# Kernel tuning notes

Hardware: AMD Instinct MI355X
Metric: run time of the kernel (lower is better)

The kernel has to match this reference:

```python
import jax, jax.numpy as jnp
import numpy as np

B, N, H = 32, 2048, 128


def _lstm_step(c, h, x, Wi, Wh, b):
    # flax LSTMCell: gates i,f,g,o; sigmoid/sigmoid/tanh/sigmoid
    gates = x @ Wi + h @ Wh + b  # (B,N,4H)
    i, f, g, o = jnp.split(gates, 4, axis=-1)
    c_new = jax.nn.sigmoid(f) * c + jax.nn.sigmoid(i) * jnp.tanh(g)
    h_new = jax.nn.sigmoid(o) * jnp.tanh(c_new)
    return c_new, h_new


def setup_inputs() -> dict:
    key = jax.random.key(0)
    ks = jax.random.split(key, 24)
    f32 = jnp.float32
    inp = {}
    inp['node_embeddings'] = jax.random.normal(ks[0], (B, N, H), f32)
    for nm, k in zip(['hs_c0', 'hs_h0', 'hs_c1', 'hs_h1'], ks[1:5]):
        inp[nm] = jax.random.normal(k, (B, N, H), f32)
    ip = jax.random.uniform(ks[5], (B, N), f32)
    inp['instruction_pointer'] = ip / jnp.sum(ip, axis=-1, keepdims=True)
    inp['Wi0'] = jax.random.normal(ks[6], (H, 4 * H), f32) * 0.05
    inp['Wh0'] = jax.random.normal(ks[7], (H, 4 * H), f32) * 0.05
    inp['b0'] = jnp.zeros((4 * H,), f32)
    inp['Wi1'] = jax.random.normal(ks[8], (H, 4 * H), f32) * 0.05
    inp['Wh1'] = jax.random.normal(ks[9], (H, 4 * H), f32) * 0.05
    inp['b1'] = jnp.zeros((4 * H,), f32)
    inp['W_raise'] = jax.random.normal(ks[10], (4 * H, 2), f32) * 0.05
    inp['b_raise'] = jnp.zeros((2,), f32)
    inp['W_branch'] = jax.random.normal(ks[11], (4 * H, 2), f32) * 0.05
    inp['b_branch'] = jnp.zeros((2,), f32)
    inp['true_indexes'] = jax.random.randint(ks[12], (B, N), 0, N, jnp.int32)
    inp['false_indexes'] = jax.random.randint(ks[13], (B, N), 0, N, jnp.int32)
    inp['raise_indexes'] = jax.random.randint(ks[14], (B, N), 0, N, jnp.int32)
    inp['exit_node_indexes'] = jax.random.randint(ks[15], (B,), 0, N, jnp.int32)
    inp['raise_node_indexes'] = jax.random.randint(ks[16], (B,), 0, N, jnp.int32)
    inp['step_limits'] = jax.random.randint(ks[17], (B,), 0, 100, jnp.int32)
    inp['current_step'] = 5
    return inp


def reference(node_embeddings, hs_c0, hs_h0, hs_c1, hs_h1, instruction_pointer,
              Wi0, Wh0, b0, Wi1, Wh1, b1, W_raise, b_raise, W_branch, b_branch,
              true_indexes, false_indexes, raise_indexes,
              exit_node_indexes, raise_node_indexes, step_limits, current_step):
    bidx = jnp.arange(B)
    old = [hs_c0, hs_h0, hs_c1, hs_h1]

    # execute: per-node 2-layer stacked LSTM (vectorized over B,N)
    c0n, h0n = _lstm_step(hs_c0, hs_h0, node_embeddings, Wi0, Wh0, b0)
    c1n, h1n = _lstm_step(hs_c1, hs_h1, h0n, Wi1, Wh1, b1)
    contrib = [c0n, h0n, c1n, h1n]

    # mask_h: keep old state at exit node and (raise_in_ipagnn) at raise node
    def mask_nodes(hc, ho, idx):
        return hc.at[bidx, idx].set(ho[bidx, idx])
    contrib = [mask_nodes(mask_nodes(hc, ho, exit_node_indexes), ho, raise_node_indexes)
               for hc, ho in zip(contrib, old)]

    hs_emb = jnp.concatenate(contrib, axis=-1)  # (B,N,4H)

    raise_dec = jax.nn.softmax(hs_emb @ W_raise + b_raise, axis=-1)
    zero_one = jnp.array([0.0, 1.0], dtype=raise_dec.dtype)
    raise_dec = raise_dec.at[bidx, exit_node_indexes].set(zero_one)
    raise_dec = raise_dec.at[bidx, raise_node_indexes].set(zero_one)
    branch_dec = jax.nn.softmax(hs_emb @ W_branch + b_branch, axis=-1)

    p_raise = raise_dec[..., 0]
    p_noraise = raise_dec[..., 1]
    p_true = p_noraise * branch_dec[..., 0]
    p_false = p_noraise * branch_dec[..., 1]

    seg = jax.vmap(lambda v, idx: jax.ops.segment_sum(v, idx, num_segments=N))
    ip = instruction_pointer
    ip_new = (seg(p_raise * ip, raise_indexes)
              + seg(p_true * ip, true_indexes)
              + seg(p_false * ip, false_indexes))  # (B,N)
    denom = (ip_new + 1e-7)[..., None]

    wr = (p_raise * ip)[..., None]
    wt = (p_true * ip)[..., None]
    wf = (p_false * ip)[..., None]

    def agg(h):
        return (seg(h * wr, raise_indexes) + seg(h * wt, true_indexes)
                + seg(h * wf, false_indexes)) / denom
    hs_new = [agg(h) for h in contrib]

    # keep_old_if_done
    not_done = (current_step < step_limits)  # (B,)
    hs_out = [jnp.where(not_done[:, None, None], hn, ho) for hn, ho in zip(hs_new, old)]
    ip_out = jnp.where(not_done[:, None], ip_new, ip)

    # pack carry: (c0,h0,c1,h1, instruction_pointer) -> (B,N,4H+1)
    return jnp.concatenate(hs_out + [ip_out[..., None]], axis=-1)
```

## Files before the change

kernel.cpp:

```cpp
#include <hip/hip_runtime.h>
#include <stdint.h>

#define BB 32
#define NN 2048
#define HH 128
#define BN (BB*NN)

typedef short v8s __attribute__((ext_vector_type(8)));
typedef float v4f __attribute__((ext_vector_type(4)));

__device__ __forceinline__ unsigned short f2b(float f){
  union { float f; unsigned int i; } v; v.f = f;
  unsigned int x = v.i;
  unsigned int r = x + 0x7FFFu + ((x >> 16) & 1u);
  return (unsigned short)(r >> 16);
}
__device__ __forceinline__ unsigned int pk2(float a, float b){
  return (unsigned int)f2b(a) | ((unsigned int)f2b(b) << 16);
}
__device__ __forceinline__ float frcp(float x){ return __builtin_amdgcn_rcpf(x); }
__device__ __forceinline__ float fsigm(float x){ return frcp(1.0f + __expf(-x)); }
__device__ __forceinline__ float ftanh(float x){ return 1.0f - 2.0f*frcp(1.0f + __expf(2.0f*x)); }

__global__ void kswz(const float* __restrict__ Wi0, const float* __restrict__ Wh0,
                     const float* __restrict__ Wi1, const float* __restrict__ Wh1,
                     unsigned short* __restrict__ Bsw0, unsigned short* __restrict__ Bsw1){
  int bid = blockIdx.x;
  int layer = bid >> 8;
  int kc = (bid >> 5) & 7;
  int ct = bid & 31;
  int lane = threadIdx.x;
  const float* Wi = layer ? Wi1 : Wi0;
  const float* Wh = layer ? Wh1 : Wh0;
  unsigned short* dst = layer ? Bsw1 : Bsw0;
  int col = ct*16 + (lane & 15);
  int kbase = kc*32 + (lane >> 4)*8;
  size_t o = ((size_t)(kc*32 + ct)*64 + (size_t)lane)*8;
  #pragma unroll
  for (int j = 0; j < 8; j++){
    int k = kbase + j;
    dst[o + j] = f2b((k < 128) ? Wi[k*512 + col] : Wh[(k-128)*512 + col]);
  }
}

__global__ void ksave(const float* __restrict__ c0, const float* __restrict__ h0,
                      const float* __restrict__ c1, const float* __restrict__ h1,
                      const int* __restrict__ exit_idx, const int* __restrict__ raise_idx,
                      float* __restrict__ saved){
  int b = blockIdx.x, which = blockIdx.y, c = threadIdx.x;
  int idx = which ? raise_idx[b] : exit_idx[b];
  size_t row = (size_t)b*NN + idx;
  const float* bufs[4] = {c0, h0, c1, h1};
  saved[((size_t)b*2 + which)*512 + c] = bufs[c >> 7][row*128 + (c & 127)];
}

__global__ void krestore(float* c0, float* h0, float* c1, float* h1,
                         const int* __restrict__ exit_idx, const int* __restrict__ raise_idx,
                         const float* __restrict__ saved){
  int b = blockIdx.x, which = blockIdx.y, c = threadIdx.x;
  int idx = which ? raise_idx[b] : exit_idx[b];
  size_t row = (size_t)b*NN + idx;
  float* bufs[4] = {c0, h0, c1, h1};
  bufs[c >> 7][row*128 + (c & 127)] = saved[((size_t)b*2 + which)*512 + c];
}

#define ROWSB 32
#define PA 264
#define PH 136

__global__ __launch_bounds__(512, 4) void klstm2(
    const float* __restrict__ ne,
    float* __restrict__ c0, float* __restrict__ h0,
    float* __restrict__ c1, float* __restrict__ h1,
    const unsigned short* __restrict__ Bsw0, const float* __restrict__ b0,
    const unsigned short* __restrict__ Bsw1, const float* __restrict__ b1,
    const int* __restrict__ step_limits, const int* __restrict__ cur_step)
{
  __shared__ unsigned short ldsA[ROWSB*PA];
  __shared__ unsigned short ldsH[ROWSB*PH];
  __shared__ unsigned short ldsG[ROWSB*PH];

  int rowbase = blockIdx.x * ROWSB;
  int b = rowbase >> 11;
  if (cur_step[0] >= step_limits[b]) return;

  int tid = threadIdx.x;
  int wid = tid >> 6, lane = tid & 63;
  int quad = lane >> 4, l16 = lane & 15;
  int ch = wid*16 + l16;

  #pragma unroll
  for (int p = 0; p < 4; p++){
    int idx = p*512 + tid;
    int row = idx >> 6, chunk = idx & 63;
    size_t g = (size_t)(rowbase + row)*128 + (chunk & 31)*4;
    float4 v = (chunk < 32) ? *(const float4*)(ne + g) : *(const float4*)(h0 + g);
    uint2 w; w.x = pk2(v.x, v.y); w.y = pk2(v.z, v.w);
    *(uint2*)&ldsA[row*PA + chunk*4] = w;
  }
  __syncthreads();

  float cpre[8], bias[4];
  #pragma unroll
  for (int rt = 0; rt < 2; rt++)
    #pragma unroll
    for (int r = 0; r < 4; r++)
      cpre[rt*4+r] = c0[((size_t)rowbase + rt*16 + quad*4 + r)*128 + ch];
  #pragma unroll
  for (int g = 0; g < 4; g++) bias[g] = b0[g*128 + ch];

  #pragma unroll
  for (int p = 0; p < 2; p++){
    int idx = p*512 + tid;
    int row = idx >> 5, chunk = idx & 31;
    float4 v = *(const float4*)(h1 + (size_t)(rowbase + row)*128 + chunk*4);
    uint2 w; w.x = pk2(v.x, v.y); w.y = pk2(v.z, v.w);
    *(uint2*)&ldsH[row*PH + chunk*4] = w;
  }

  const v8s* Bv0 = (const v8s*)Bsw0;
  v4f acc[2][4] = {};
  v8s bc[4], bn[4];
  #pragma unroll
  for (int g = 0; g < 4; g++) bc[g] = Bv0[(size_t)(g*8 + wid)*64 + lane];
  #pragma unroll
  for (int kc = 0; kc < 8; kc++){
    if (kc < 7){
      #pragma unroll
      for (int g = 0; g < 4; g++) bn[g] = Bv0[(size_t)((kc+1)*32 + g*8 + wid)*64 + lane];
    }
    v8s a0 = *(const v8s*)&ldsA[(0*16 + l16)*PA + kc*32 + quad*8];
    v8s a1 = *(const v8s*)&ldsA[(1*16 + l16)*PA + kc*32 + quad*8];
    #pragma unroll
    for (int g = 0; g < 4; g++){
      acc[0][g] = __builtin_amdgcn_mfma_f32_16x16x32_bf16(a0, bc[g], acc[0][g], 0,0,0);
      acc[1][g] = __builtin_amdgcn_mfma_f32_16x16x32_bf16(a1, bc[g], acc[1][g], 0,0,0);
    }
    #pragma unroll
    for (int g = 0; g < 4; g++) bc[g] = bn[g];
  }

  #pragma unroll
  for (int rt = 0; rt < 2; rt++){
    #pragma unroll
    for (int r = 0; r < 4; r++){
      int lrow = rt*16 + quad*4 + r;
      size_t row = (size_t)rowbase + lrow;
      float iv = acc[rt][0][r] + bias[0];
      float fv = acc[rt][1][r] + bias[1];
      float gv = acc[rt][2][r] + bias[2];
      float ov = acc[rt][3][r] + bias[3];
      float cold = cpre[rt*4+r];
      float cn = fsigm(fv)*cold + fsigm(iv)*ftanh(gv);
      float hn = fsigm(ov)*ftanh(cn);
      c0[row*128 + ch] = cn;
      h0[row*128 + ch] = hn;
      ldsG[lrow*PH + ch] = f2b(hn);
    }
  }
  __syncthreads();

  #pragma unroll
  for (int rt = 0; rt < 2; rt++)
    #pragma unroll
    for (int r = 0; r < 4; r++)
      cpre[rt*4+r] = c1[((size_t)rowbase + rt*16 + quad*4 + r)*128 + ch];
  #pragma unroll
  for (int g = 0; g < 4; g++) bias[g] = b1[g*128 + ch];

  const v8s* Bv1 = (const v8s*)Bsw1;
  #pragma unroll
  for (int rt = 0; rt < 2; rt++)
    #pragma unroll
    for (int g = 0; g < 4; g++)
      acc[rt][g] = (v4f){0.f, 0.f, 0.f, 0.f};
  #pragma unroll
  for (int g = 0; g < 4; g++) bc[g] = Bv1[(size_t)(g*8 + wid)*64 + lane];
  #pragma unroll
  for (int kc = 0; kc < 8; kc++){
    if (kc < 7){
      #pragma unroll
      for (int g = 0; g < 4; g++) bn[g] = Bv1[(size_t)((kc+1)*32 + g*8 + wid)*64 + lane];
    }
    v8s a0, a1;
    if (kc < 4){
      a0 = *(const v8s*)&ldsG[(0*16 + l16)*PH + kc*32 + quad*8];
      a1 = *(const v8s*)&ldsG[(1*16 + l16)*PH + kc*32 + quad*8];
    } else {
      a0 = *(const v8s*)&ldsH[(0*16 + l16)*PH + (kc-4)*32 + quad*8];
      a1 = *(const v8s*)&ldsH[(1*16 + l16)*PH + (kc-4)*32 + quad*8];
    }
    #pragma unroll
    for (int g = 0; g < 4; g++){
      acc[0][g] = __builtin_amdgcn_mfma_f32_16x16x32_bf16(a0, bc[g], acc[0][g], 0,0,0);
      acc[1][g] = __builtin_amdgcn_mfma_f32_16x16x32_bf16(a1, bc[g], acc[1][g], 0,0,0);
    }
    #pragma unroll
    for (int g = 0; g < 4; g++) bc[g] = bn[g];
  }

  #pragma unroll
  for (int rt = 0; rt < 2; rt++){
    #pragma unroll
    for (int r = 0; r < 4; r++){
      size_t row = (size_t)rowbase + rt*16 + quad*4 + r;
      float iv = acc[rt][0][r] + bias[0];
      float fv = acc[rt][1][r] + bias[1];
      float gv = acc[rt][2][r] + bias[2];
      float ov = acc[rt][3][r] + bias[3];
      float cold = cpre[rt*4+r];
      float cn = fsigm(fv)*cold + fsigm(iv)*ftanh(gv);
      float hn = fsigm(ov)*ftanh(cn);
      c1[row*128 + ch] = cn;
      h1[row*128 + ch] = hn;
    }
  }
}

__global__ __launch_bounds__(256) void kdec(
    const float* __restrict__ c0, const float* __restrict__ h0,
    const float* __restrict__ c1, const float* __restrict__ h1,
    const float* __restrict__ Wr, const float* __restrict__ br,
    const float* __restrict__ Wb, const float* __restrict__ bb,
    const float* __restrict__ ip,
    const int* __restrict__ exit_idx, const int* __restrict__ raise_idx,
    const int* __restrict__ ri, const int* __restrict__ ti, const int* __restrict__ fi,
    int* __restrict__ counts,
    float* __restrict__ wbuf)
{
  int tid = threadIdx.x;
  int wid = tid >> 6, lane = tid & 63;
  int gid = blockIdx.x*4 + wid;
  int b = gid >> 11, n = gid & 2047;

  const float* bufs[4] = {c0, h0, c1, h1};
  const float* hb = bufs[lane >> 4] + (size_t)gid*128 + (lane & 15)*8;
  float4 hv0 = *(const float4*)hb;
  float4 hv1 = *(const float4*)(hb + 4);
  float hv[8] = {hv0.x, hv0.y, hv0.z, hv0.w, hv1.x, hv1.y, hv1.z, hv1.w};
  const float* wrp = Wr + lane*16;
  const float* wbp = Wb + lane*16;
  float r0=0.f, r1=0.f, q0=0.f, q1=0.f;
  #pragma unroll
  for (int j = 0; j < 8; j++){
    float h = hv[j];
    r0 += h * wrp[j*2];  r1 += h * wrp[j*2+1];
    q0 += h * wbp[j*2];  q1 += h * wbp[j*2+1];
  }
  #pragma unroll
  for (int off = 32; off > 0; off >>= 1){
    r0 += __shfl_xor(r0, off, 64);
    r1 += __shfl_xor(r1, off, 64);
    q0 += __shfl_xor(q0, off, 64);
    q1 += __shfl_xor(q1, off, 64);
  }
  if (lane == 0){
    r0 += br[0]; r1 += br[1];
    q0 += bb[0]; q1 += bb[1];
    float pr, pn;
    if (n == exit_idx[b] || n == raise_idx[b]){ pr = 0.f; pn = 1.f; }
    else {
      float m = fmaxf(r0, r1);
      float e0 = __expf(r0 - m), e1 = __expf(r1 - m);
      pr = e0 / (e0 + e1); pn = e1 / (e0 + e1);
    }
    float m2 = fmaxf(q0, q1);
    float f0 = __expf(q0 - m2), f1 = __expf(q1 - m2);
    float pt = f0 / (f0 + f1), pf = f1 / (f0 + f1);
    float ipv = ip[gid];
    wbuf[0*BN + gid] = pr * ipv;
    wbuf[1*BN + gid] = pn * pt * ipv;
    wbuf[2*BN + gid] = pn * pf * ipv;
  } else if (lane == 1){
    atomicAdd(&counts[(b<<11) + ri[gid]], 1);
  } else if (lane == 2){
    atomicAdd(&counts[(b<<11) + ti[gid]], 1);
  } else if (lane == 3){
    atomicAdd(&counts[(b<<11) + fi[gid]], 1);
  }
}

__global__ __launch_bounds__(256) void kscan(const int* __restrict__ counts,
                                             int* __restrict__ offsets){
  __shared__ int lds[256];
  int b = blockIdx.x, tid = threadIdx.x;
  const int* c = counts + b*NN;
  int* o = offsets + b*NN;
  int v[8]; int s = 0;
  #pragma unroll
  for (int i = 0; i < 8; i++){ v[i] = c[tid*8+i]; s += v[i]; }
  lds[tid] = s;
  __syncthreads();
  if (tid == 0){
    int run = 0;
    for (int t = 0; t < 256; t++){ int tmp = lds[t]; lds[t] = run; run += tmp; }
  }
  __syncthreads();
  int off = lds[tid];
  #pragma unroll
  for (int i = 0; i < 8; i++){ o[tid*8+i] = off; off += v[i]; }
}

__global__ void kfill(const int* __restrict__ ri, const int* __restrict__ ti,
                      const int* __restrict__ fi, const int* __restrict__ offsets,
                      int* __restrict__ cursor, unsigned short* __restrict__ edges){
  int gid = blockIdx.x*256 + threadIdx.x;
  int b = gid >> 11, n = gid & 2047;
  size_t ebase = (size_t)b*3*NN;
  int t0 = ri[gid]; int p0 = atomicAdd(&cursor[b*NN+t0], 1);
  edges[ebase + offsets[b*NN+t0] + p0] = (unsigned short)(n);
  int t1 = ti[gid]; int p1 = atomicAdd(&cursor[b*NN+t1], 1);
  edges[ebase + offsets[b*NN+t1] + p1] = (unsigned short)(n | (1<<11));
  int t2 = fi[gid]; int p2 = atomicAdd(&cursor[b*NN+t2], 1);
  edges[ebase + offsets[b*NN+t2] + p2] = (unsigned short)(n | (2<<11));
}

__global__ __launch_bounds__(128) void kagg(
    const float* __restrict__ c0, const float* __restrict__ h0,
    const float* __restrict__ c1, const float* __restrict__ h1,
    const float* __restrict__ ip,
    const float* __restrict__ wbuf, const unsigned short* __restrict__ edges,
    const int* __restrict__ counts, const int* __restrict__ offsets,
    const int* __restrict__ step_limits, const int* __restrict__ cur_step,
    float* __restrict__ out)
{
  int gid = blockIdx.x;
  int b = gid >> 11;
  int tid = threadIdx.x;
  size_t obase = (size_t)gid*513;
  const float* bufs[4] = {c0, h0, c1, h1};

  if (cur_step[0] >= step_limits[b]){
    int c = tid*4;
    const float* s = bufs[c >> 7];
    size_t rb = (size_t)gid*128 + (c & 127);
    out[obase + c+0] = s[rb+0];
    out[obase + c+1] = s[rb+1];
    out[obase + c+2] = s[rb+2];
    out[obase + c+3] = s[rb+3];
    if (tid == 0) out[obase + 512] = ip[gid];
    return;
  }

  int cnt = counts[gid], off = offsets[gid];
  const unsigned short* eb = edges + (size_t)b*3*NN + off;
  const float* sb = bufs[tid >> 5];
  int coff = (tid & 31)*4;
  float a0=0.f, a1=0.f, a2=0.f, a3=0.f, ipn=0.f;
  for (int e = 0; e < cnt; e++){
    int pk = eb[e];
    int n = pk & 2047, et = pk >> 11;
    float w = wbuf[et*BN + (b<<11) + n];
    ipn += w;
    float4 sv = *(const float4*)(sb + ((size_t)(b<<11) + n)*128 + coff);
    a0 += w * sv.x;
    a1 += w * sv.y;
    a2 += w * sv.z;
    a3 += w * sv.w;
  }
  int c = tid*4;
  float inv = 1.0f / (ipn + 1e-7f);
  out[obase + c+0] = a0*inv;
  out[obase + c+1] = a1*inv;
  out[obase + c+2] = a2*inv;
  out[obase + c+3] = a3*inv;
  if (tid == 0) out[obase + 512] = ipn;
}

extern "C" void kernel_launch(void* const* d_in, const int* in_sizes, int n_in,
                              void* d_out, int out_size, void* d_ws, size_t ws_size,
                              hipStream_t stream){
  const float* ne  = (const float*)d_in[0];
  float* c0  = (float*)d_in[1];
  float* h0  = (float*)d_in[2];
  float* c1  = (float*)d_in[3];
  float* h1  = (float*)d_in[4];
  const float* ip  = (const float*)d_in[5];
  const float* Wi0 = (const float*)d_in[6];
  const float* Wh0 = (const float*)d_in[7];
  const float* b0  = (const float*)d_in[8];
  const float* Wi1 = (const float*)d_in[9];
  const float* Wh1 = (const float*)d_in[10];
  const float* b1  = (const float*)d_in[11];
  const float* Wr  = (const float*)d_in[12];
  const float* br  = (const float*)d_in[13];
  const float* Wb  = (const float*)d_in[14];
  const float* bb  = (const float*)d_in[15];
  const int* ti  = (const int*)d_in[16];
  const int* fi  = (const int*)d_in[17];
  const int* ri  = (const int*)d_in[18];
  const int* ei  = (const int*)d_in[19];
  const int* rni = (const int*)d_in[20];
  const int* sl  = (const int*)d_in[21];
  const int* cs  = (const int*)d_in[22];
  float* out = (float*)d_out;

  uint8_t* ws = (uint8_t*)d_ws;
  unsigned short* Bsw0    = (unsigned short*)(ws + 0);
  unsigned short* Bsw1    = (unsigned short*)(ws + 262144);
  float*          saved   = (float*)(ws + 524288);
  float*          wbuf    = (float*)(ws + 655360);
  int*            counts  = (int*)(ws + 1441792);
  int*            offsets = (int*)(ws + 1703936);
  int*            cursor  = (int*)(ws + 1966080);
  unsigned short* edges   = (unsigned short*)(ws + 2228224);

  hipMemsetAsync(counts, 0, BN*sizeof(int), stream);
  hipMemsetAsync(cursor, 0, BN*sizeof(int), stream);

  kswz<<<512, 64, 0, stream>>>(Wi0, Wh0, Wi1, Wh1, Bsw0, Bsw1);
  ksave<<<dim3(BB, 2), 512, 0, stream>>>(c0, h0, c1, h1, ei, rni, saved);

  klstm2<<<BN/ROWSB, 512, 0, stream>>>(ne, c0, h0, c1, h1, Bsw0, b0, Bsw1, b1, sl, cs);

  krestore<<<dim3(BB, 2), 512, 0, stream>>>(c0, h0, c1, h1, ei, rni, saved);

  kdec<<<BN/4, 256, 0, stream>>>(c0, h0, c1, h1, Wr, br, Wb, bb, ip, ei, rni,
                                 ri, ti, fi, counts, wbuf);

  kscan<<<BB, 256, 0, stream>>>(counts, offsets);
  kfill<<<BN/256, 256, 0, stream>>>(ri, ti, fi, offsets, cursor, edges);

  kagg<<<BN, 128, 0, stream>>>(c0, h0, c1, h1, ip, wbuf, edges, counts, offsets,
                               sl, cs, out);
}
```

Measured before the change: 463.5 us.

## Fuse decision heads and edge counting into LSTM kernel, drop save/restore passes

```diff
diff --git a/kernel.cpp b/kernel.cpp
--- a/kernel.cpp
+++ b/kernel.cpp
@@ -43,27 +43,6 @@
   }
 }
 
-__global__ void ksave(const float* __restrict__ c0, const float* __restrict__ h0,
-                      const float* __restrict__ c1, const float* __restrict__ h1,
-                      const int* __restrict__ exit_idx, const int* __restrict__ raise_idx,
-                      float* __restrict__ saved){
-  int b = blockIdx.x, which = blockIdx.y, c = threadIdx.x;
-  int idx = which ? raise_idx[b] : exit_idx[b];
-  size_t row = (size_t)b*NN + idx;
-  const float* bufs[4] = {c0, h0, c1, h1};
-  saved[((size_t)b*2 + which)*512 + c] = bufs[c >> 7][row*128 + (c & 127)];
-}
-
-__global__ void krestore(float* c0, float* h0, float* c1, float* h1,
-                         const int* __restrict__ exit_idx, const int* __restrict__ raise_idx,
-                         const float* __restrict__ saved){
-  int b = blockIdx.x, which = blockIdx.y, c = threadIdx.x;
-  int idx = which ? raise_idx[b] : exit_idx[b];
-  size_t row = (size_t)b*NN + idx;
-  float* bufs[4] = {c0, h0, c1, h1};
-  bufs[c >> 7][row*128 + (c & 127)] = saved[((size_t)b*2 + which)*512 + c];
-}
-
 #define ROWSB 32
 #define PA 264
 #define PH 136
@@ -74,11 +53,19 @@
     float* __restrict__ c1, float* __restrict__ h1,
     const unsigned short* __restrict__ Bsw0, const float* __restrict__ b0,
     const unsigned short* __restrict__ Bsw1, const float* __restrict__ b1,
+    const float* __restrict__ Wr, const float* __restrict__ br,
+    const float* __restrict__ Wb, const float* __restrict__ bb,
+    const float* __restrict__ ip,
+    const int* __restrict__ exit_idx, const int* __restrict__ raise_idx,
+    const int* __restrict__ ri, const int* __restrict__ ti, const int* __restrict__ fi,
+    int* __restrict__ counts,
+    float* __restrict__ wbuf,
     const int* __restrict__ step_limits, const int* __restrict__ cur_step)
 {
   __shared__ unsigned short ldsA[ROWSB*PA];
   __shared__ unsigned short ldsH[ROWSB*PH];
   __shared__ unsigned short ldsG[ROWSB*PH];
+  __shared__ float ldsR[ROWSB*8*4];
 
   int rowbase = blockIdx.x * ROWSB;
   int b = rowbase >> 11;
@@ -88,6 +75,7 @@
   int wid = tid >> 6, lane = tid & 63;
   int quad = lane >> 4, l16 = lane & 15;
   int ch = wid*16 + l16;
+  int e_row = exit_idx[b], r_row = raise_idx[b];
 
   #pragma unroll
   for (int p = 0; p < 4; p++){
@@ -98,17 +86,6 @@
     uint2 w; w.x = pk2(v.x, v.y); w.y = pk2(v.z, v.w);
     *(uint2*)&ldsA[row*PA + chunk*4] = w;
   }
-  __syncthreads();
-
-  float cpre[8], bias[4];
-  #pragma unroll
-  for (int rt = 0; rt < 2; rt++)
-    #pragma unroll
-    for (int r = 0; r < 4; r++)
-      cpre[rt*4+r] = c0[((size_t)rowbase + rt*16 + quad*4 + r)*128 + ch];
-  #pragma unroll
-  for (int g = 0; g < 4; g++) bias[g] = b0[g*128 + ch];
-
   #pragma unroll
   for (int p = 0; p < 2; p++){
     int idx = p*512 + tid;
@@ -118,11 +95,22 @@
     *(uint2*)&ldsH[row*PH + chunk*4] = w;
   }
 
+  float cpre[8], bias[4];
+  #pragma unroll
+  for (int rt = 0; rt < 2; rt++)
+    #pragma unroll
+    for (int r = 0; r < 4; r++)
+      cpre[rt*4+r] = c0[((size_t)rowbase + rt*16 + quad*4 + r)*128 + ch];
+  #pragma unroll
+  for (int g = 0; g < 4; g++) bias[g] = b0[g*128 + ch];
   const v8s* Bv0 = (const v8s*)Bsw0;
+  v8s bc[4], bn[4];
+  #pragma unroll
+  for (int g = 0; g < 4; g++) bc[g] = Bv0[(size_t)(g*8 + wid)*64 + lane];
+
+  __syncthreads();
+
   v4f acc[2][4] = {};
-  v8s bc[4], bn[4];
-  #pragma unroll
-  for (int g = 0; g < 4; g++) bc[g] = Bv0[(size_t)(g*8 + wid)*64 + lane];
   #pragma unroll
   for (int kc = 0; kc < 8; kc++){
     if (kc < 7){
@@ -140,25 +128,30 @@
     for (int g = 0; g < 4; g++) bc[g] = bn[g];
   }
 
+  float cn0[8], hn0[8];
   #pragma unroll
   for (int rt = 0; rt < 2; rt++){
     #pragma unroll
     for (int r = 0; r < 4; r++){
+      int k = rt*4 + r;
       int lrow = rt*16 + quad*4 + r;
-      size_t row = (size_t)rowbase + lrow;
+      int grow = rowbase + lrow;
+      int node = grow & 2047;
+      bool special = (node == e_row) || (node == r_row);
       float iv = acc[rt][0][r] + bias[0];
       float fv = acc[rt][1][r] + bias[1];
       float gv = acc[rt][2][r] + bias[2];
       float ov = acc[rt][3][r] + bias[3];
-      float cold = cpre[rt*4+r];
-      float cn = fsigm(fv)*cold + fsigm(iv)*ftanh(gv);
+      float cn = fsigm(fv)*cpre[k] + fsigm(iv)*ftanh(gv);
       float hn = fsigm(ov)*ftanh(cn);
-      c0[row*128 + ch] = cn;
-      h0[row*128 + ch] = hn;
+      cn0[k] = cn; hn0[k] = hn;
+      if (!special){
+        c0[(size_t)grow*128 + ch] = cn;
+        h0[(size_t)grow*128 + ch] = hn;
+      }
       ldsG[lrow*PH + ch] = f2b(hn);
     }
   }
-  __syncthreads();
 
   #pragma unroll
   for (int rt = 0; rt < 2; rt++)
@@ -167,15 +160,17 @@
       cpre[rt*4+r] = c1[((size_t)rowbase + rt*16 + quad*4 + r)*128 + ch];
   #pragma unroll
   for (int g = 0; g < 4; g++) bias[g] = b1[g*128 + ch];
-
   const v8s* Bv1 = (const v8s*)Bsw1;
+  #pragma unroll
+  for (int g = 0; g < 4; g++) bc[g] = Bv1[(size_t)(g*8 + wid)*64 + lane];
+
+  __syncthreads();
+
   #pragma unroll
   for (int rt = 0; rt < 2; rt++)
     #pragma unroll
     for (int g = 0; g < 4; g++)
       acc[rt][g] = (v4f){0.f, 0.f, 0.f, 0.f};
-  #pragma unroll
-  for (int g = 0; g < 4; g++) bc[g] = Bv1[(size_t)(g*8 + wid)*64 + lane];
   #pragma unroll
   for (int kc = 0; kc < 8; kc++){
     if (kc < 7){
@@ -199,96 +194,131 @@
     for (int g = 0; g < 4; g++) bc[g] = bn[g];
   }
 
+  float2 wrA = *(const float2*)&Wr[(      ch)*2];
+  float2 wrB = *(const float2*)&Wr[(128 + ch)*2];
+  float2 wrC = *(const float2*)&Wr[(256 + ch)*2];
+  float2 wrD = *(const float2*)&Wr[(384 + ch)*2];
+  float2 wbA = *(const float2*)&Wb[(      ch)*2];
+  float2 wbB = *(const float2*)&Wb[(128 + ch)*2];
+  float2 wbC = *(const float2*)&Wb[(256 + ch)*2];
+  float2 wbD = *(const float2*)&Wb[(384 + ch)*2];
+
   #pragma unroll
   for (int rt = 0; rt < 2; rt++){
     #pragma unroll
     for (int r = 0; r < 4; r++){
-      size_t row = (size_t)rowbase + rt*16 + quad*4 + r;
+      int k = rt*4 + r;
+      int lrow = rt*16 + quad*4 + r;
+      int grow = rowbase + lrow;
+      int node = grow & 2047;
+      bool special = (node == e_row) || (node == r_row);
       float iv = acc[rt][0][r] + bias[0];
       float fv = acc[rt][1][r] + bias[1];
       float gv = acc[rt][2][r] + bias[2];
       float ov = acc[rt][3][r] + bias[3];
-      float cold = cpre[rt*4+r];
-      float cn = fsigm(fv)*cold + fsigm(iv)*ftanh(gv);
+      float cn = fsigm(fv)*cpre[k] + fsigm(iv)*ftanh(gv);
       float hn = fsigm(ov)*ftanh(cn);
-      c1[row*128 + ch] = cn;
-      h1[row*128 + ch] = hn;
-    }
-  }
-}
-
-__global__ __launch_bounds__(256) void kdec(
+      if (!special){
+        c1[(size_t)grow*128 + ch] = cn;
+        h1[(size_t)grow*128 + ch] = hn;
+      }
+      float p0 = cn0[k]*wrA.x + hn0[k]*wrB.x + cn*wrC.x + hn*wrD.x;
+      float p1 = cn0[k]*wrA.y + hn0[k]*wrB.y + cn*wrC.y + hn*wrD.y;
+      float p2 = cn0[k]*wbA.x + hn0[k]*wbB.x + cn*wbC.x + hn*wbD.x;
+      float p3 = cn0[k]*wbA.y + hn0[k]*wbB.y + cn*wbC.y + hn*wbD.y;
+      #pragma unroll
+      for (int off = 1; off < 16; off <<= 1){
+        p0 += __shfl_xor(p0, off, 64);
+        p1 += __shfl_xor(p1, off, 64);
+        p2 += __shfl_xor(p2, off, 64);
+        p3 += __shfl_xor(p3, off, 64);
+      }
+      if (l16 == 0){
+        float4 pv = {p0, p1, p2, p3};
+        *(float4*)&ldsR[(lrow*8 + wid)*4] = pv;
+      }
+    }
+  }
+  __syncthreads();
+
+  if (tid < 32){
+    int grow = rowbase + tid;
+    float s0=0.f, s1=0.f, s2=0.f, s3=0.f;
+    #pragma unroll
+    for (int w = 0; w < 8; w++){
+      float4 pv = *(const float4*)&ldsR[(tid*8 + w)*4];
+      s0 += pv.x; s1 += pv.y; s2 += pv.z; s3 += pv.w;
+    }
+    float r0 = s0 + br[0], r1 = s1 + br[1];
+    float q0 = s2 + bb[0], q1 = s3 + bb[1];
+    float m = fmaxf(r0, r1);
+    float e0 = __expf(r0 - m), e1 = __expf(r1 - m);
+    float pr = e0 / (e0 + e1), pn = e1 / (e0 + e1);
+    float m2 = fmaxf(q0, q1);
+    float f0 = __expf(q0 - m2), f1 = __expf(q1 - m2);
+    float pt = f0 / (f0 + f1), pf = f1 / (f0 + f1);
+    float ipv = ip[grow];
+    wbuf[0*BN + grow] = pr * ipv;
+    wbuf[1*BN + grow] = pn * pt * ipv;
+    wbuf[2*BN + grow] = pn * pf * ipv;
+    atomicAdd(&counts[(b<<11) + ri[grow]], 1);
+    atomicAdd(&counts[(b<<11) + ti[grow]], 1);
+    atomicAdd(&counts[(b<<11) + fi[grow]], 1);
+  }
+}
+
+__global__ __launch_bounds__(64) void kpatch(
     const float* __restrict__ c0, const float* __restrict__ h0,
     const float* __restrict__ c1, const float* __restrict__ h1,
-    const float* __restrict__ Wr, const float* __restrict__ br,
     const float* __restrict__ Wb, const float* __restrict__ bb,
     const float* __restrict__ ip,
     const int* __restrict__ exit_idx, const int* __restrict__ raise_idx,
-    const int* __restrict__ ri, const int* __restrict__ ti, const int* __restrict__ fi,
-    int* __restrict__ counts,
     float* __restrict__ wbuf)
 {
-  int tid = threadIdx.x;
-  int wid = tid >> 6, lane = tid & 63;
-  int gid = blockIdx.x*4 + wid;
-  int b = gid >> 11, n = gid & 2047;
-
+  int b = blockIdx.x;
+  int idx = blockIdx.y ? raise_idx[b] : exit_idx[b];
+  int gid = (b << 11) + idx;
+  int lane = threadIdx.x;
   const float* bufs[4] = {c0, h0, c1, h1};
   const float* hb = bufs[lane >> 4] + (size_t)gid*128 + (lane & 15)*8;
   float4 hv0 = *(const float4*)hb;
   float4 hv1 = *(const float4*)(hb + 4);
   float hv[8] = {hv0.x, hv0.y, hv0.z, hv0.w, hv1.x, hv1.y, hv1.z, hv1.w};
-  const float* wrp = Wr + lane*16;
   const float* wbp = Wb + lane*16;
-  float r0=0.f, r1=0.f, q0=0.f, q1=0.f;
+  float q0=0.f, q1=0.f;
   #pragma unroll
   for (int j = 0; j < 8; j++){
-    float h = hv[j];
-    r0 += h * wrp[j*2];  r1 += h * wrp[j*2+1];
-    q0 += h * wbp[j*2];  q1 += h * wbp[j*2+1];
+    q0 += hv[j] * wbp[j*2];
+    q1 += hv[j] * wbp[j*2+1];
   }
   #pragma unroll
   for (int off = 32; off > 0; off >>= 1){
-    r0 += __shfl_xor(r0, off, 64);
-    r1 += __shfl_xor(r1, off, 64);
     q0 += __shfl_xor(q0, off, 64);
     q1 += __shfl_xor(q1, off, 64);
   }
   if (lane == 0){
-    r0 += br[0]; r1 += br[1];
     q0 += bb[0]; q1 += bb[1];
-    float pr, pn;
-    if (n == exit_idx[b] || n == raise_idx[b]){ pr = 0.f; pn = 1.f; }
-    else {
-      float m = fmaxf(r0, r1);
-      float e0 = __expf(r0 - m), e1 = __expf(r1 - m);
-      pr = e0 / (e0 + e1); pn = e1 / (e0 + e1);
-    }
     float m2 = fmaxf(q0, q1);
     float f0 = __expf(q0 - m2), f1 = __expf(q1 - m2);
     float pt = f0 / (f0 + f1), pf = f1 / (f0 + f1);
     float ipv = ip[gid];
-    wbuf[0*BN + gid] = pr * ipv;
-    wbuf[1*BN + gid] = pn * pt * ipv;
-    wbuf[2*BN + gid] = pn * pf * ipv;
-  } else if (lane == 1){
-    atomicAdd(&counts[(b<<11) + ri[gid]], 1);
-  } else if (lane == 2){
-    atomicAdd(&counts[(b<<11) + ti[gid]], 1);
-  } else if (lane == 3){
-    atomicAdd(&counts[(b<<11) + fi[gid]], 1);
+    wbuf[0*BN + gid] = 0.f;
+    wbuf[1*BN + gid] = pt * ipv;
+    wbuf[2*BN + gid] = pf * ipv;
   }
 }
 
 __global__ __launch_bounds__(256) void kscan(const int* __restrict__ counts,
-                                             int* __restrict__ offsets){
+                                             int* __restrict__ offsets,
+                                             int* __restrict__ cursor){
   __shared__ int lds[256];
   int b = blockIdx.x, tid = threadIdx.x;
   const int* c = counts + b*NN;
   int* o = offsets + b*NN;
+  int* cu = cursor + b*NN;
   int v[8]; int s = 0;
   #pragma unroll
-  for (int i = 0; i < 8; i++){ v[i] = c[tid*8+i]; s += v[i]; }
+  for (int i = 0; i < 8; i++){ v[i] = c[tid*8+i]; s += v[i]; cu[tid*8+i] = 0; }
   lds[tid] = s;
   __syncthreads();
   if (tid == 0){
@@ -398,7 +428,6 @@
   uint8_t* ws = (uint8_t*)d_ws;
   unsigned short* Bsw0    = (unsigned short*)(ws + 0);
   unsigned short* Bsw1    = (unsigned short*)(ws + 262144);
-  float*          saved   = (float*)(ws + 524288);
   float*          wbuf    = (float*)(ws + 655360);
   int*            counts  = (int*)(ws + 1441792);
   int*            offsets = (int*)(ws + 1703936);
@@ -406,19 +435,16 @@
   unsigned short* edges   = (unsigned short*)(ws + 2228224);
 
   hipMemsetAsync(counts, 0, BN*sizeof(int), stream);
-  hipMemsetAsync(cursor, 0, BN*sizeof(int), stream);
 
   kswz<<<512, 64, 0, stream>>>(Wi0, Wh0, Wi1, Wh1, Bsw0, Bsw1);
-  ksave<<<dim3(BB, 2), 512, 0, stream>>>(c0, h0, c1, h1, ei, rni, saved);
-
-  klstm2<<<BN/ROWSB, 512, 0, stream>>>(ne, c0, h0, c1, h1, Bsw0, b0, Bsw1, b1, sl, cs);
-
-  krestore<<<dim3(BB, 2), 512, 0, stream>>>(c0, h0, c1, h1, ei, rni, saved);
-
-  kdec<<<BN/4, 256, 0, stream>>>(c0, h0, c1, h1, Wr, br, Wb, bb, ip, ei, rni,
-                                 ri, ti, fi, counts, wbuf);
-
-  kscan<<<BB, 256, 0, stream>>>(counts, offsets);
+
+  klstm2<<<BN/ROWSB, 512, 0, stream>>>(ne, c0, h0, c1, h1, Bsw0, b0, Bsw1, b1,
+                                       Wr, br, Wb, bb, ip, ei, rni,
+                                       ri, ti, fi, counts, wbuf, sl, cs);
+
+  kpatch<<<dim3(BB, 2), 64, 0, stream>>>(c0, h0, c1, h1, Wb, bb, ip, ei, rni, wbuf);
+
+  kscan<<<BB, 256, 0, stream>>>(counts, offsets, cursor);
   kfill<<<BN/256, 256, 0, stream>>>(ri, ti, fi, offsets, cursor, edges);
 
   kagg<<<BN, 128, 0, stream>>>(c0, h0, c1, h1, ip, wbuf, edges, counts, offsets,
```

New measurement: 451.0 us. 1.03x faster.

## Store LSTM states as bf16 scratch and drop save/restore kernels

Applied to the files above, without the earlier changes.

```diff
diff --git a/kernel.cpp b/kernel.cpp
--- a/kernel.cpp
+++ b/kernel.cpp
@@ -17,6 +17,9 @@
 }
 __device__ __forceinline__ unsigned int pk2(float a, float b){
   return (unsigned int)f2b(a) | ((unsigned int)f2b(b) << 16);
+}
+__device__ __forceinline__ float b2f(unsigned int s){
+  union { unsigned int i; float f; } v; v.i = s << 16; return v.f;
 }
 __device__ __forceinline__ float frcp(float x){ return __builtin_amdgcn_rcpf(x); }
 __device__ __forceinline__ float fsigm(float x){ return frcp(1.0f + __expf(-x)); }
@@ -43,27 +46,6 @@
   }
 }
 
-__global__ void ksave(const float* __restrict__ c0, const float* __restrict__ h0,
-                      const float* __restrict__ c1, const float* __restrict__ h1,
-                      const int* __restrict__ exit_idx, const int* __restrict__ raise_idx,
-                      float* __restrict__ saved){
-  int b = blockIdx.x, which = blockIdx.y, c = threadIdx.x;
-  int idx = which ? raise_idx[b] : exit_idx[b];
-  size_t row = (size_t)b*NN + idx;
-  const float* bufs[4] = {c0, h0, c1, h1};
-  saved[((size_t)b*2 + which)*512 + c] = bufs[c >> 7][row*128 + (c & 127)];
-}
-
-__global__ void krestore(float* c0, float* h0, float* c1, float* h1,
-                         const int* __restrict__ exit_idx, const int* __restrict__ raise_idx,
-                         const float* __restrict__ saved){
-  int b = blockIdx.x, which = blockIdx.y, c = threadIdx.x;
-  int idx = which ? raise_idx[b] : exit_idx[b];
-  size_t row = (size_t)b*NN + idx;
-  float* bufs[4] = {c0, h0, c1, h1};
-  bufs[c >> 7][row*128 + (c & 127)] = saved[((size_t)b*2 + which)*512 + c];
-}
-
 #define ROWSB 32
 #define PA 264
 #define PH 136
@@ -72,9 +54,13 @@
     const float* __restrict__ ne,
     float* __restrict__ c0, float* __restrict__ h0,
     float* __restrict__ c1, float* __restrict__ h1,
+    unsigned short* __restrict__ sc0, unsigned short* __restrict__ sh0,
+    unsigned short* __restrict__ sc1, unsigned short* __restrict__ sh1,
     const unsigned short* __restrict__ Bsw0, const float* __restrict__ b0,
     const unsigned short* __restrict__ Bsw1, const float* __restrict__ b1,
-    const int* __restrict__ step_limits, const int* __restrict__ cur_step)
+    const int* __restrict__ exit_idx, const int* __restrict__ raise_idx,
+    const int* __restrict__ step_limits, const int* __restrict__ cur_step,
+    int useb)
 {
   __shared__ unsigned short ldsA[ROWSB*PA];
   __shared__ unsigned short ldsH[ROWSB*PH];
@@ -88,6 +74,7 @@
   int wid = tid >> 6, lane = tid & 63;
   int quad = lane >> 4, l16 = lane & 15;
   int ch = wid*16 + l16;
+  int e_row = exit_idx[b], r_row = raise_idx[b];
 
   #pragma unroll
   for (int p = 0; p < 4; p++){
@@ -144,21 +131,27 @@
   for (int rt = 0; rt < 2; rt++){
     #pragma unroll
     for (int r = 0; r < 4; r++){
+      int k = rt*4 + r;
       int lrow = rt*16 + quad*4 + r;
-      size_t row = (size_t)rowbase + lrow;
+      int grow = rowbase + lrow;
+      int node = grow & 2047;
+      bool special = (node == e_row) || (node == r_row);
       float iv = acc[rt][0][r] + bias[0];
       float fv = acc[rt][1][r] + bias[1];
       float gv = acc[rt][2][r] + bias[2];
       float ov = acc[rt][3][r] + bias[3];
-      float cold = cpre[rt*4+r];
-      float cn = fsigm(fv)*cold + fsigm(iv)*ftanh(gv);
+      float cn = fsigm(fv)*cpre[k] + fsigm(iv)*ftanh(gv);
       float hn = fsigm(ov)*ftanh(cn);
-      c0[row*128 + ch] = cn;
-      h0[row*128 + ch] = hn;
+      if (useb){
+        sc0[(size_t)grow*128 + ch] = special ? f2b(cpre[k]) : f2b(cn);
+        sh0[(size_t)grow*128 + ch] = special ? ldsA[lrow*PA + 128 + ch] : f2b(hn);
+      } else if (!special){
+        c0[(size_t)grow*128 + ch] = cn;
+        h0[(size_t)grow*128 + ch] = hn;
+      }
       ldsG[lrow*PH + ch] = f2b(hn);
     }
   }
-  __syncthreads();
 
   #pragma unroll
   for (int rt = 0; rt < 2; rt++)
@@ -167,15 +160,17 @@
       cpre[rt*4+r] = c1[((size_t)rowbase + rt*16 + quad*4 + r)*128 + ch];
   #pragma unroll
   for (int g = 0; g < 4; g++) bias[g] = b1[g*128 + ch];
-
   const v8s* Bv1 = (const v8s*)Bsw1;
+  #pragma unroll
+  for (int g = 0; g < 4; g++) bc[g] = Bv1[(size_t)(g*8 + wid)*64 + lane];
+
+  __syncthreads();
+
   #pragma unroll
   for (int rt = 0; rt < 2; rt++)
     #pragma unroll
     for (int g = 0; g < 4; g++)
       acc[rt][g] = (v4f){0.f, 0.f, 0.f, 0.f};
-  #pragma unroll
-  for (int g = 0; g < 4; g++) bc[g] = Bv1[(size_t)(g*8 + wid)*64 + lane];
   #pragma unroll
   for (int kc = 0; kc < 8; kc++){
     if (kc < 7){
@@ -203,16 +198,24 @@
   for (int rt = 0; rt < 2; rt++){
     #pragma unroll
     for (int r = 0; r < 4; r++){
-      size_t row = (size_t)rowbase + rt*16 + quad*4 + r;
+      int k = rt*4 + r;
+      int lrow = rt*16 + quad*4 + r;
+      int grow = rowbase + lrow;
+      int node = grow & 2047;
+      bool special = (node == e_row) || (node == r_row);
       float iv = acc[rt][0][r] + bias[0];
       float fv = acc[rt][1][r] + bias[1];
       float gv = acc[rt][2][r] + bias[2];
       float ov = acc[rt][3][r] + bias[3];
-      float cold = cpre[rt*4+r];
-      float cn = fsigm(fv)*cold + fsigm(iv)*ftanh(gv);
+      float cn = fsigm(fv)*cpre[k] + fsigm(iv)*ftanh(gv);
       float hn = fsigm(ov)*ftanh(cn);
-      c1[row*128 + ch] = cn;
-      h1[row*128 + ch] = hn;
+      if (useb){
+        sc1[(size_t)grow*128 + ch] = special ? f2b(cpre[k]) : f2b(cn);
+        sh1[(size_t)grow*128 + ch] = special ? ldsH[lrow*PH + ch] : f2b(hn);
+      } else if (!special){
+        c1[(size_t)grow*128 + ch] = cn;
+        h1[(size_t)grow*128 + ch] = hn;
+      }
     }
   }
 }
@@ -220,24 +223,38 @@
 __global__ __launch_bounds__(256) void kdec(
     const float* __restrict__ c0, const float* __restrict__ h0,
     const float* __restrict__ c1, const float* __restrict__ h1,
+    const unsigned short* __restrict__ sc0, const unsigned short* __restrict__ sh0,
+    const unsigned short* __restrict__ sc1, const unsigned short* __restrict__ sh1,
     const float* __restrict__ Wr, const float* __restrict__ br,
     const float* __restrict__ Wb, const float* __restrict__ bb,
     const float* __restrict__ ip,
     const int* __restrict__ exit_idx, const int* __restrict__ raise_idx,
     const int* __restrict__ ri, const int* __restrict__ ti, const int* __restrict__ fi,
     int* __restrict__ counts,
-    float* __restrict__ wbuf)
+    float* __restrict__ wbuf, int useb)
 {
   int tid = threadIdx.x;
   int wid = tid >> 6, lane = tid & 63;
   int gid = blockIdx.x*4 + wid;
   int b = gid >> 11, n = gid & 2047;
 
-  const float* bufs[4] = {c0, h0, c1, h1};
-  const float* hb = bufs[lane >> 4] + (size_t)gid*128 + (lane & 15)*8;
-  float4 hv0 = *(const float4*)hb;
-  float4 hv1 = *(const float4*)(hb + 4);
-  float hv[8] = {hv0.x, hv0.y, hv0.z, hv0.w, hv1.x, hv1.y, hv1.z, hv1.w};
+  float hv[8];
+  if (useb){
+    const unsigned short* bufs16[4] = {sc0, sh0, sc1, sh1};
+    const unsigned short* hb = bufs16[lane >> 4] + (size_t)gid*128 + (lane & 15)*8;
+    uint4 raw = *(const uint4*)hb;
+    hv[0] = b2f(raw.x & 0xffffu); hv[1] = b2f(raw.x >> 16);
+    hv[2] = b2f(raw.y & 0xffffu); hv[3] = b2f(raw.y >> 16);
+    hv[4] = b2f(raw.z & 0xffffu); hv[5] = b2f(raw.z >> 16);
+    hv[6] = b2f(raw.w & 0xffffu); hv[7] = b2f(raw.w >> 16);
+  } else {
+    const float* bufs[4] = {c0, h0, c1, h1};
+    const float* hb = bufs[lane >> 4] + (size_t)gid*128 + (lane & 15)*8;
+    float4 hv0 = *(const float4*)hb;
+    float4 hv1 = *(const float4*)(hb + 4);
+    hv[0]=hv0.x; hv[1]=hv0.y; hv[2]=hv0.z; hv[3]=hv0.w;
+    hv[4]=hv1.x; hv[5]=hv1.y; hv[6]=hv1.z; hv[7]=hv1.w;
+  }
   const float* wrp = Wr + lane*16;
   const float* wbp = Wb + lane*16;
   float r0=0.f, r1=0.f, q0=0.f, q1=0.f;
@@ -281,14 +298,16 @@
 }
 
 __global__ __launch_bounds__(256) void kscan(const int* __restrict__ counts,
-                                             int* __restrict__ offsets){
+                                             int* __restrict__ offsets,
+                                             int* __restrict__ cursor){
   __shared__ int lds[256];
   int b = blockIdx.x, tid = threadIdx.x;
   const int* c = counts + b*NN;
   int* o = offsets + b*NN;
+  int* cu = cursor + b*NN;
   int v[8]; int s = 0;
   #pragma unroll
-  for (int i = 0; i < 8; i++){ v[i] = c[tid*8+i]; s += v[i]; }
+  for (int i = 0; i < 8; i++){ v[i] = c[tid*8+i]; s += v[i]; cu[tid*8+i] = 0; }
   lds[tid] = s;
   __syncthreads();
   if (tid == 0){
@@ -318,11 +337,13 @@
 __global__ __launch_bounds__(128) void kagg(
     const float* __restrict__ c0, const float* __restrict__ h0,
     const float* __restrict__ c1, const float* __restrict__ h1,
+    const unsigned short* __restrict__ sc0, const unsigned short* __restrict__ sh0,
+    const unsigned short* __restrict__ sc1, const unsigned short* __restrict__ sh1,
     const float* __restrict__ ip,
     const float* __restrict__ wbuf, const unsigned short* __restrict__ edges,
     const int* __restrict__ counts, const int* __restrict__ offsets,
     const int* __restrict__ step_limits, const int* __restrict__ cur_step,
-    float* __restrict__ out)
+    float* __restrict__ out, int useb)
 {
   int gid = blockIdx.x;
   int b = gid >> 11;
@@ -344,19 +365,38 @@
 
   int cnt = counts[gid], off = offsets[gid];
   const unsigned short* eb = edges + (size_t)b*3*NN + off;
-  const float* sb = bufs[tid >> 5];
   int coff = (tid & 31)*4;
   float a0=0.f, a1=0.f, a2=0.f, a3=0.f, ipn=0.f;
-  for (int e = 0; e < cnt; e++){
-    int pk = eb[e];
-    int n = pk & 2047, et = pk >> 11;
-    float w = wbuf[et*BN + (b<<11) + n];
-    ipn += w;
-    float4 sv = *(const float4*)(sb + ((size_t)(b<<11) + n)*128 + coff);
-    a0 += w * sv.x;
-    a1 += w * sv.y;
-    a2 += w * sv.z;
-    a3 += w * sv.w;
+  int pk = (cnt > 0) ? eb[0] : 0;
+  if (useb){
+    const unsigned short* bufs16[4] = {sc0, sh0, sc1, sh1};
+    const unsigned short* sb = bufs16[tid >> 5];
+    for (int e = 0; e < cnt; e++){
+      int pkn = (e+1 < cnt) ? eb[e+1] : 0;
+      int n = pk & 2047, et = pk >> 11;
+      float w = wbuf[et*BN + (b<<11) + n];
+      uint2 raw = *(const uint2*)(sb + ((size_t)(b<<11) + n)*128 + coff);
+      ipn += w;
+      a0 += w * b2f(raw.x & 0xffffu);
+      a1 += w * b2f(raw.x >> 16);
+      a2 += w * b2f(raw.y & 0xffffu);
+      a3 += w * b2f(raw.y >> 16);
+      pk = pkn;
+    }
+  } else {
+    const float* sb = bufs[tid >> 5];
+    for (int e = 0; e < cnt; e++){
+      int pkn = (e+1 < cnt) ? eb[e+1] : 0;
+      int n = pk & 2047, et = pk >> 11;
+      float w = wbuf[et*BN + (b<<11) + n];
+      float4 sv = *(const float4*)(sb + ((size_t)(b<<11) + n)*128 + coff);
+      ipn += w;
+      a0 += w * sv.x;
+      a1 += w * sv.y;
+      a2 += w * sv.z;
+      a3 += w * sv.w;
+      pk = pkn;
+    }
   }
   int c = tid*4;
   float inv = 1.0f / (ipn + 1e-7f);
@@ -398,29 +438,36 @@
   uint8_t* ws = (uint8_t*)d_ws;
   unsigned short* Bsw0    = (unsigned short*)(ws + 0);
   unsigned short* Bsw1    = (unsigned short*)(ws + 262144);
-  float*          saved   = (float*)(ws + 524288);
   float*          wbuf    = (float*)(ws + 655360);
   int*            counts  = (int*)(ws + 1441792);
   int*            offsets = (int*)(ws + 1703936);
   int*            cursor  = (int*)(ws + 1966080);
   unsigned short* edges   = (unsigned short*)(ws + 2228224);
+  const size_t SBASE = 2621440;
+  const size_t SB    = (size_t)BN * 128 * 2;
+  int useb = (ws_size >= SBASE + 4*SB) ? 1 : 0;
+  unsigned short* sc0 = (unsigned short*)(ws + SBASE + 0*SB);
+  unsigned short* sh0 = (unsigned short*)(ws + SBASE + 1*SB);
+  unsigned short* sc1 = (unsigned short*)(ws + SBASE + 2*SB);
+  unsigned short* sh1 = (unsigned short*)(ws + SBASE + 3*SB);
 
   hipMemsetAsync(counts, 0, BN*sizeof(int), stream);
-  hipMemsetAsync(cursor, 0, BN*sizeof(int), stream);
 
   kswz<<<512, 64, 0, stream>>>(Wi0, Wh0, Wi1, Wh1, Bsw0, Bsw1);
-  ksave<<<dim3(BB, 2), 512, 0, stream>>>(c0, h0, c1, h1, ei, rni, saved);
-
-  klstm2<<<BN/ROWSB, 512, 0, stream>>>(ne, c0, h0, c1, h1, Bsw0, b0, Bsw1, b1, sl, cs);
-
-  krestore<<<dim3(BB, 2), 512, 0, stream>>>(c0, h0, c1, h1, ei, rni, saved);
-
-  kdec<<<BN/4, 256, 0, stream>>>(c0, h0, c1, h1, Wr, br, Wb, bb, ip, ei, rni,
-                                 ri, ti, fi, counts, wbuf);
-
-  kscan<<<BB, 256, 0, stream>>>(counts, offsets);
+
+  klstm2<<<BN/ROWSB, 512, 0, stream>>>(ne, c0, h0, c1, h1,
+                                       sc0, sh0, sc1, sh1,
+                                       Bsw0, b0, Bsw1, b1,
+                                       ei, rni, sl, cs, useb);
+
+  kdec<<<BN/4, 256, 0, stream>>>(c0, h0, c1, h1, sc0, sh0, sc1, sh1,
+                                 Wr, br, Wb, bb, ip, ei, rni,
+                                 ri, ti, fi, counts, wbuf, useb);
+
+  kscan<<<BB, 256, 0, stream>>>(counts, offsets, cursor);
   kfill<<<BN/256, 256, 0, stream>>>(ri, ti, fi, offsets, cursor, edges);
 
-  kagg<<<BN, 128, 0, stream>>>(c0, h0, c1, h1, ip, wbuf, edges, counts, offsets,
-                               sl, cs, out);
-}
+  kagg<<<BN, 128, 0, stream>>>(c0, h0, c1, h1, sc0, sh0, sc1, sh1,
+                               ip, wbuf, edges, counts, offsets,
+                               sl, cs, out, useb);
+}
```

New measurement: 441.4 us. 4.8% less time.
